# Performance work log

Measured on AMD Instinct MI355X. Metric: run time of the kernel, lower is better.

## Reference

```python
import jax, jax.numpy as jnp
import numpy as np

EMBED_DIM = 256
NUM_HEADS = 8
NB = 8          # number of scenes (batches)
LQ = 256        # queries per scene
LS = 4096       # source points per scene
LN_EPS = 1e-5


def setup_inputs() -> dict:
    key = jax.random.key(0)
    ks = jax.random.split(key, 8)
    d = EMBED_DIM
    n_q, n_s = NB * LQ, NB * LS
    w_scale = d ** -0.5  # xavier-ish
    return {
        "source": jax.random.normal(ks[0], (n_s, d), jnp.float32),
        "query": jax.random.normal(ks[1], (n_q, d), jnp.float32),
        "source_pe": 0.1 * jax.random.normal(ks[2], (n_s, d), jnp.float32),
        "query_pe": 0.1 * jax.random.normal(ks[3], (n_q, d), jnp.float32),
        "in_proj_w": w_scale * jax.random.normal(ks[4], (3 * d, d), jnp.float32),
        "in_proj_b": jnp.zeros((3 * d,), jnp.float32),
        "out_w": w_scale * jax.random.normal(ks[5], (d, d), jnp.float32),
        "out_b": jnp.zeros((d,), jnp.float32),
        "ln_w": jnp.ones((d,), jnp.float32),
        "ln_b": jnp.zeros((d,), jnp.float32),
        # sorted equal-size segments: token i belongs to scene i // L
        "source_batch": (jnp.arange(n_s, dtype=jnp.int32) // LS).astype(jnp.int32),
        "query_batch": (jnp.arange(n_q, dtype=jnp.int32) // LQ).astype(jnp.int32),
        "B": NB,
    }


def reference(source, query, source_pe, query_pe, in_proj_w, in_proj_b,
              out_w, out_b, ln_w, ln_b, source_batch, query_batch, B):
    d = source.shape[-1]
    H = NUM_HEADS
    hd = d // H
    Lq = query.shape[0] // B
    Ls = source.shape[0] // B

    # batch ids are sorted equal segments -> per-scene gather == reshape
    q_in = (query + query_pe).reshape(B, Lq, d)   # q with pos embed
    k_in = (source + source_pe).reshape(B, Ls, d) # k with pos embed
    v_in = source.reshape(B, Ls, d)               # v without pos embed

    Wq, Wk, Wv = jnp.split(in_proj_w, 3, axis=0)
    bq, bk, bv = jnp.split(in_proj_b, 3)

    q = (q_in @ Wq.T + bq).reshape(B, Lq, H, hd)
    k = (k_in @ Wk.T + bk).reshape(B, Ls, H, hd)
    v = (v_in @ Wv.T + bv).reshape(B, Ls, H, hd)

    scores = jnp.einsum('bqhd,bkhd->bhqk', q, k) * (hd ** -0.5)
    attn = jax.nn.softmax(scores, axis=-1)
    o = jnp.einsum('bhqk,bkhd->bqhd', attn, v).reshape(B, Lq, d)
    o = o @ out_w.T + out_b

    # residual (dropout is identity at p=0) + LayerNorm
    res = o + query.reshape(B, Lq, d)
    mu = jnp.mean(res, axis=-1, keepdims=True)
    var = jnp.var(res, axis=-1, keepdims=True)
    y = (res - mu) * jax.lax.rsqrt(var + LN_EPS) * ln_w + ln_b
    return y.reshape(-1, d)
```

## Files before the change

kernel.cpp:

```cpp
#include <hip/hip_runtime.h>
#include <hip/hip_bf16.h>

typedef __bf16 bf16;
typedef __bf16 bf16x4 __attribute__((ext_vector_type(4)));
typedef __bf16 bf16x8 __attribute__((ext_vector_type(8)));
typedef float f32x4 __attribute__((ext_vector_type(4)));

#define D 256
#define NHEAD 8
#define HD 32
#define NB_ 8
#define LQ_ 256
#define LS_ 4096
#define MQ (NB_ * LQ_)
#define MS (NB_ * LS_)

#define QSCALE 0.25500527f

__global__ __launch_bounds__(256) void prep(
    const float* __restrict__ source, const float* __restrict__ source_pe,
    const float* __restrict__ query, const float* __restrict__ query_pe,
    const float* __restrict__ w_in, const float* __restrict__ w_out,
    bf16* __restrict__ SPb, bf16* __restrict__ QPb, bf16* __restrict__ Wb)
{
    const int NS4 = MS * D / 4;
    const int NQ4 = MQ * D / 4;
    const int NW4 = (768 * 256 + 256 * 256) / 4;
    const int total = NS4 + NQ4 + NW4;
    for (int i = blockIdx.x * 256 + threadIdx.x; i < total; i += gridDim.x * 256) {
        if (i < NS4) {
            const float4 s = ((const float4*)source)[i];
            const float4 p = ((const float4*)source_pe)[i];
            bf16x4 osp;
            osp[0] = (bf16)(s.x + p.x); osp[1] = (bf16)(s.y + p.y);
            osp[2] = (bf16)(s.z + p.z); osp[3] = (bf16)(s.w + p.w);
            ((bf16x4*)SPb)[i] = osp;
        } else if (i < NS4 + NQ4) {
            const int j = i - NS4;
            const float4 s = ((const float4*)query)[j];
            const float4 p = ((const float4*)query_pe)[j];
            bf16x4 o;
            o[0] = (bf16)(s.x + p.x); o[1] = (bf16)(s.y + p.y);
            o[2] = (bf16)(s.z + p.z); o[3] = (bf16)(s.w + p.w);
            ((bf16x4*)QPb)[j] = o;
        } else {
            const int j = i - NS4 - NQ4;
            const float4 v = (j < 49152) ? ((const float4*)w_in)[j]
                                         : ((const float4*)w_out)[j - 49152];
            bf16x4 o;
            o[0] = (bf16)v.x; o[1] = (bf16)v.y; o[2] = (bf16)v.z; o[3] = (bf16)v.w;
            ((bf16x4*)Wb)[j] = o;
        }
    }
}

__global__ __launch_bounds__(256, 4) void gemm_proj(
    const bf16* __restrict__ SPb, const float* __restrict__ srcf,
    const bf16* __restrict__ QPb, const bf16* __restrict__ Wb,
    const float* __restrict__ in_proj_b,
    bf16* __restrict__ Kt, bf16* __restrict__ Vt2, bf16* __restrict__ Qb)
{
    __shared__ __align__(16) bf16 smem[2][128][72];
    bf16 (*As)[72] = smem[0];
    bf16 (*Bs)[72] = smem[1];
    const int tid = threadIdx.x, lane = tid & 63, wid = tid >> 6;
    const int wm = wid >> 1, wn = wid & 1;
    const int g = lane >> 4, q15 = lane & 15;
    const int id = blockIdx.x;

    const bf16* A; const bf16* W; const float* bias; bf16* out;
    int omode, mblk, nblk;
    if (id < 512) {
        A = SPb; W = Wb + 256 * D; bias = in_proj_b + 256; out = Kt;
        mblk = id >> 1; nblk = id & 1; omode = 1;
    } else if (id < 1024) {
        A = nullptr; W = Wb + 512 * D; bias = in_proj_b + 512; out = Vt2;
        mblk = (id - 512) >> 1; nblk = id & 1; omode = 2;
    } else {
        A = QPb; W = Wb; bias = in_proj_b; out = Qb;
        mblk = (id - 1024) >> 1; nblk = id & 1; omode = 0;
    }

    f32x4 acc[4][4];
    #pragma unroll
    for (int i = 0; i < 4; ++i)
        #pragma unroll
        for (int j = 0; j < 4; ++j) acc[i][j] = (f32x4){0.f, 0.f, 0.f, 0.f};

    const size_t arow0 = (size_t)mblk * 128;
    const int brow0 = nblk * 128;

    for (int kk = 0; kk < 4; ++kk) {
        const int d0 = kk * 64;
        if (omode == 2) {
            #pragma unroll
            for (int i = 0; i < 8; ++i) {
                const int idx = i * 256 + tid;
                const int r = idx >> 4, c = (idx & 15) * 4;
                const float4 v = *(const float4*)&srcf[(arow0 + r) * D + d0 + c];
                bf16x4 o;
                o[0] = (bf16)v.x; o[1] = (bf16)v.y; o[2] = (bf16)v.z; o[3] = (bf16)v.w;
                *(bf16x4*)&As[r][c] = o;
            }
            #pragma unroll
            for (int i = 0; i < 4; ++i) {
                const int idx = i * 256 + tid;
                const int r = idx >> 3, c = (idx & 7) * 8;
                *(bf16x8*)&Bs[r][c] = *(const bf16x8*)&W[(size_t)(brow0 + r) * D + d0 + c];
            }
        } else {
            #pragma unroll
            for (int i = 0; i < 4; ++i) {
                const int idx = i * 256 + tid;
                const int r = idx >> 3, c = (idx & 7) * 8;
                *(bf16x8*)&As[r][c] = *(const bf16x8*)&A[(arow0 + r) * D + d0 + c];
                *(bf16x8*)&Bs[r][c] = *(const bf16x8*)&W[(size_t)(brow0 + r) * D + d0 + c];
            }
        }
        __syncthreads();
        #pragma unroll
        for (int h2 = 0; h2 < 2; ++h2) {
            const int ko = h2 * 32 + g * 8;
            bf16x8 af[4], bfr[4];
            #pragma unroll
            for (int i = 0; i < 4; ++i)
                af[i] = *(const bf16x8*)&As[wm * 64 + i * 16 + q15][ko];
            #pragma unroll
            for (int j = 0; j < 4; ++j)
                bfr[j] = *(const bf16x8*)&Bs[wn * 64 + j * 16 + q15][ko];
            #pragma unroll
            for (int i = 0; i < 4; ++i)
                #pragma unroll
                for (int j = 0; j < 4; ++j)
                    acc[i][j] = __builtin_amdgcn_mfma_f32_16x16x32_bf16(
                        af[i], bfr[j], acc[i][j], 0, 0, 0);
        }
        __syncthreads();
    }

    if (omode == 0) {
        #pragma unroll
        for (int i = 0; i < 4; ++i)
            #pragma unroll
            for (int j = 0; j < 4; ++j) {
                const int n_g = nblk * 128 + wn * 64 + j * 16 + q15;
                const float b = bias[n_g];
                #pragma unroll
                for (int r = 0; r < 4; ++r) {
                    const size_t m_g = arow0 + wm * 64 + i * 16 + g * 4 + r;
                    out[m_g * D + n_g] = (bf16)((acc[i][j][r] + b) * QSCALE);
                }
            }
    } else if (omode == 1) {
        bf16* Ls = &smem[0][0][0];
        #pragma unroll
        for (int i = 0; i < 4; ++i)
            #pragma unroll
            for (int j = 0; j < 4; ++j) {
                const int n_loc = wn * 64 + j * 16 + q15;
                const int h_loc = n_loc >> 5, d = n_loc & 31;
                const int gp = d >> 3, e = d & 7;
                const float b = bias[nblk * 128 + n_loc];
                #pragma unroll
                for (int r = 0; r < 4; ++r) {
                    const int m_loc = wm * 64 + i * 16 + g * 4 + r;
                    const int c_loc = m_loc >> 6, kl = m_loc & 63;
                    const int t = ((kl >> 5) << 1) | ((kl >> 2) & 1);
                    const int q15p = ((kl >> 3) & 3) * 4 + (kl & 3);
                    Ls[(h_loc * 2 + c_loc) * 2048 + t * 512
                       + (gp * 16 + q15p) * 8 + e] = (bf16)(acc[i][j][r] + b);
                }
            }
        __syncthreads();
        const int bb = (int)(arow0 >> 12);
        const int c0 = (int)((arow0 & 4095) >> 6);
        const int h0 = (nblk * 128) >> 5;
        #pragma unroll
        for (int p = 0; p < 8; ++p) {
            const int idx = p * 2048 + tid * 8;
            const int blk = idx >> 11, within = idx & 2047;
            *(bf16x8*)&out[((size_t)(bb * 8 + h0 + (blk >> 1)) * 64
                            + c0 + (blk & 1)) * 2048 + within]
                = *(const bf16x8*)&Ls[idx];
        }
    } else {
        #pragma unroll
        for (int i = 0; i < 4; ++i)
            #pragma unroll
            for (int j = 0; j < 4; ++j) {
                const int n_g = nblk * 128 + wn * 64 + j * 16 + q15;
                const int h = n_g >> 5, d = n_g & 31;
                const int dt = d >> 4, q15p = d & 15;
                const float b = bias[n_g];
                const size_t m_g0 = arow0 + wm * 64 + i * 16 + g * 4;
                const int bb = (int)(m_g0 >> 12);
                const int c = (int)((m_g0 & 4095) >> 6);
                const int kl0 = (int)(m_g0 & 63);
                const int half = kl0 >> 5, gp = (kl0 >> 3) & 3, e0 = kl0 & 7;
                const int f = dt * 2 + half;
                bf16x4 o;
                #pragma unroll
                for (int r = 0; r < 4; ++r) o[r] = (bf16)(acc[i][j][r] + b);
                *(bf16x4*)&out[((size_t)(bb * 8 + h) * 64 + c) * 2048
                               + f * 512 + (gp * 16 + q15p) * 8 + e0] = o;
            }
    }
}

template<int S>
__global__ __launch_bounds__(256, 2) void attn_kernel(
    const bf16* __restrict__ Qb, const bf16* __restrict__ Kt,
    const bf16* __restrict__ Vt2,
    bf16* __restrict__ accp, float* __restrict__ lp)
{
    const int tid = threadIdx.x, lane = tid & 63, wid = tid >> 6;
    const int q15 = lane & 15, g = lane >> 4;
    const int bid = blockIdx.x;
    const int h = bid & 7;
    const int inner = bid >> 3;
    const int split = inner % S;
    const int b = inner / S;
    constexpr int CHUNKS = LS_ / S / 64;

    const int q0 = b * LQ_ + wid * 64;
    bf16x8 qf[4];
    #pragma unroll
    for (int f = 0; f < 4; ++f)
        qf[f] = *(const bf16x8*)&Qb[(size_t)(q0 + f * 16 + q15) * D + h * HD + g * 8];

    const f32x4 minit = (f32x4){-8.f, -8.f, -8.f, -8.f};
    const size_t cbase = ((size_t)(b * 8 + h) * 64 + split * CHUNKS) * 2048;
    const bf16* kp = Kt + cbase + lane * 8;
    const bf16* vp = Vt2 + cbase + lane * 8;

    float lr[4] = {0.f, 0.f, 0.f, 0.f};
    f32x4 a0[4], a1[4];
    #pragma unroll
    for (int f = 0; f < 4; ++f) {
        a0[f] = (f32x4){0.f, 0.f, 0.f, 0.f};
        a1[f] = (f32x4){0.f, 0.f, 0.f, 0.f};
    }

    for (int kc = 0; kc < CHUNKS; ++kc) {
        const size_t co = (size_t)kc * 2048;

        bf16x8 kf[4], vf[4];
        #pragma unroll
        for (int t = 0; t < 4; ++t) kf[t] = *(const bf16x8*)&kp[co + t * 512];
        #pragma unroll
        for (int t = 0; t < 4; ++t) vf[t] = *(const bf16x8*)&vp[co + t * 512];

        #pragma unroll
        for (int f = 0; f < 4; ++f) {
            f32x4 s0 = __builtin_amdgcn_mfma_f32_16x16x32_bf16(kf[0], qf[f], minit, 0, 0, 0);
            f32x4 s1 = __builtin_amdgcn_mfma_f32_16x16x32_bf16(kf[1], qf[f], minit, 0, 0, 0);
            f32x4 s2 = __builtin_amdgcn_mfma_f32_16x16x32_bf16(kf[2], qf[f], minit, 0, 0, 0);
            f32x4 s3 = __builtin_amdgcn_mfma_f32_16x16x32_bf16(kf[3], qf[f], minit, 0, 0, 0);

            bf16x8 pa0, pa1;
            #pragma unroll
            for (int r = 0; r < 4; ++r) {
                const float p0 = exp2f(s0[r]);
                const float p1 = exp2f(s1[r]);
                const float p2 = exp2f(s2[r]);
                const float p3 = exp2f(s3[r]);
                lr[f] += (p0 + p1) + (p2 + p3);
                pa0[r]     = (bf16)p0;
                pa0[4 + r] = (bf16)p1;
                pa1[r]     = (bf16)p2;
                pa1[4 + r] = (bf16)p3;
            }

            a0[f] = __builtin_amdgcn_mfma_f32_16x16x32_bf16(pa0, vf[0], a0[f], 0, 0, 0);
            a0[f] = __builtin_amdgcn_mfma_f32_16x16x32_bf16(pa1, vf[1], a0[f], 0, 0, 0);
            a1[f] = __builtin_amdgcn_mfma_f32_16x16x32_bf16(pa0, vf[2], a1[f], 0, 0, 0);
            a1[f] = __builtin_amdgcn_mfma_f32_16x16x32_bf16(pa1, vf[3], a1[f], 0, 0, 0);
        }
    }

    const int task0 = (b * 8 + h) * 16 + wid * 4;
    #pragma unroll
    for (int f = 0; f < 4; ++f) {
        lr[f] += __shfl_xor(lr[f], 16);
        lr[f] += __shfl_xor(lr[f], 32);
        const size_t base = ((size_t)((task0 + f) * S + split) * 64 + lane) * 8;
        bf16x4 o0, o1;
        #pragma unroll
        for (int r = 0; r < 4; ++r) {
            o0[r] = (bf16)a0[f][r];
            o1[r] = (bf16)a1[f][r];
        }
        *(bf16x4*)&accp[base]     = o0;
        *(bf16x4*)&accp[base + 4] = o1;
        if (lane < 16)
            lp[((task0 + f) * S + split) * 16 + lane] = lr[f];
    }
}

template<int S>
__global__ __launch_bounds__(256) void attn_combine(
    const bf16* __restrict__ accp, const float* __restrict__ lp,
    bf16* __restrict__ Ob)
{
    const int tid = threadIdx.x, lane = tid & 63, wid = tid >> 6;
    const int task = blockIdx.x * 4 + wid;
    const int g = lane >> 4, q15 = lane & 15;

    f32x4 o0 = (f32x4){0.f, 0.f, 0.f, 0.f};
    f32x4 o1 = (f32x4){0.f, 0.f, 0.f, 0.f};
    float ll = 0.f;
    #pragma unroll
    for (int s = 0; s < S; ++s) {
        const size_t base = ((size_t)(task * S + s) * 64 + lane) * 8;
        const bf16x8 v = *(const bf16x8*)&accp[base];
        #pragma unroll
        for (int r = 0; r < 4; ++r) { o0[r] += (float)v[r]; o1[r] += (float)v[4 + r]; }
        if (lane < 16) ll += lp[(task * S + s) * 16 + lane];
    }

    const int b = task >> 7, h = (task >> 4) & 7, qg = task & 15;
    #pragma unroll
    for (int r = 0; r < 4; ++r) {
        const float inv = 1.f / __shfl(ll, g * 4 + r);
        const size_t row = (size_t)b * LQ_ + qg * 16 + g * 4 + r;
        Ob[row * D + h * HD + q15]      = (bf16)(o0[r] * inv);
        Ob[row * D + h * HD + 16 + q15] = (bf16)(o1[r] * inv);
    }
}

__global__ __launch_bounds__(256) void out_ln_kernel(
    const bf16* __restrict__ Ob, const bf16* __restrict__ Wout,
    const float* __restrict__ out_b, const float* __restrict__ query,
    const float* __restrict__ lnw, const float* __restrict__ lnb,
    float* __restrict__ out)
{
    __shared__ bf16 As[32][72];
    __shared__ bf16 Bs[256][72];
    __shared__ float red[2][32][2];
    const int tid = threadIdx.x, lane = tid & 63, wid = tid >> 6;
    const int wm = wid >> 1, wn = wid & 1;
    const int g = lane >> 4, q15 = lane & 15;
    const size_t row0 = (size_t)blockIdx.x * 32;

    f32x4 acc[8];
    #pragma unroll
    for (int j = 0; j < 8; ++j) acc[j] = (f32x4){0.f, 0.f, 0.f, 0.f};

    for (int kk = 0; kk < 4; ++kk) {
        const int d0 = kk * 64;
        {
            const int r = tid >> 3, c = (tid & 7) * 8;
            *(bf16x8*)&As[r][c] = *(const bf16x8*)&Ob[(row0 + r) * D + d0 + c];
        }
        #pragma unroll
        for (int i = 0; i < 8; ++i) {
            const int idx = i * 256 + tid;
            const int r = idx >> 3, c = (idx & 7) * 8;
            *(bf16x8*)&Bs[r][c] = *(const bf16x8*)&Wout[(size_t)r * D + d0 + c];
        }
        __syncthreads();
        #pragma unroll
        for (int h2 = 0; h2 < 2; ++h2) {
            const int ko = h2 * 32 + g * 8;
            const bf16x8 af = *(const bf16x8*)&As[wm * 16 + q15][ko];
            #pragma unroll
            for (int j = 0; j < 8; ++j) {
                const bf16x8 bfr = *(const bf16x8*)&Bs[wn * 128 + j * 16 + q15][ko];
                acc[j] = __builtin_amdgcn_mfma_f32_16x16x32_bf16(af, bfr, acc[j], 0, 0, 0);
            }
        }
        __syncthreads();
    }

    float bl[8], lw[8], lbv[8];
    #pragma unroll
    for (int j = 0; j < 8; ++j) {
        const int n = wn * 128 + j * 16 + q15;
        bl[j] = out_b[n]; lw[j] = lnw[n]; lbv[j] = lnb[n];
    }

    #pragma unroll
    for (int r = 0; r < 4; ++r) {
        const int rl = wm * 16 + g * 4 + r;
        const size_t m = row0 + rl;
        float s = 0.f, sq = 0.f;
        #pragma unroll
        for (int j = 0; j < 8; ++j) {
            const float v = acc[j][r] + bl[j] + query[m * D + wn * 128 + j * 16 + q15];
            acc[j][r] = v;
            s += v; sq += v * v;
        }
        s += __shfl_xor(s, 1);  sq += __shfl_xor(sq, 1);
        s += __shfl_xor(s, 2);  sq += __shfl_xor(sq, 2);
        s += __shfl_xor(s, 4);  sq += __shfl_xor(sq, 4);
        s += __shfl_xor(s, 8);  sq += __shfl_xor(sq, 8);
        if (q15 == r) {
            red[wn][rl][0] = s;
            red[wn][rl][1] = sq;
        }
    }
    __syncthreads();

    #pragma unroll
    for (int r = 0; r < 4; ++r) {
        const int rl = wm * 16 + g * 4 + r;
        const float s  = red[0][rl][0] + red[1][rl][0];
        const float sq = red[0][rl][1] + red[1][rl][1];
        const float mean = s * (1.f / 256.f);
        const float var  = sq * (1.f / 256.f) - mean * mean;
        const float inv  = rsqrtf(var + 1e-5f);
        const size_t m = row0 + rl;
        #pragma unroll
        for (int j = 0; j < 8; ++j)
            out[m * D + wn * 128 + j * 16 + q15] =
                (acc[j][r] - mean) * inv * lw[j] + lbv[j];
    }
}

extern "C" void kernel_launch(void* const* d_in, const int* in_sizes, int n_in,
                              void* d_out, int out_size, void* d_ws, size_t ws_size,
                              hipStream_t stream) {
    (void)in_sizes; (void)n_in; (void)out_size; (void)ws_size;
    const float* source    = (const float*)d_in[0];
    const float* query     = (const float*)d_in[1];
    const float* source_pe = (const float*)d_in[2];
    const float* query_pe  = (const float*)d_in[3];
    const float* in_proj_w = (const float*)d_in[4];
    const float* in_proj_b = (const float*)d_in[5];
    const float* out_w     = (const float*)d_in[6];
    const float* out_b     = (const float*)d_in[7];
    const float* ln_w      = (const float*)d_in[8];
    const float* ln_b      = (const float*)d_in[9];

    constexpr int S = 8;
    bf16* Wb   = (bf16*)d_ws;
    bf16* QPb  = Wb + 1024 * 256;
    bf16* Qb   = QPb + (size_t)MQ * D;
    bf16* Kt   = Qb + (size_t)MQ * D;
    bf16* Vt2  = Kt + (size_t)MS * D;
    bf16* SPb  = Vt2 + (size_t)MS * D;
    bf16* Ob   = SPb + (size_t)MS * D;
    bf16* accp = Ob + (size_t)MQ * D;
    float* lp  = (float*)(accp + (size_t)1024 * S * 64 * 8);
    float* outp = (float*)d_out;

    prep<<<dim3(2048), dim3(256), 0, stream>>>(
        source, source_pe, query, query_pe, in_proj_w, out_w,
        SPb, QPb, Wb);
    gemm_proj<<<dim3(1056), dim3(256), 0, stream>>>(
        SPb, source, QPb, Wb, in_proj_b, Kt, Vt2, Qb);
    attn_kernel<S><<<dim3(512), dim3(256), 0, stream>>>(Qb, Kt, Vt2, accp, lp);
    attn_combine<S><<<dim3(256), dim3(256), 0, stream>>>(accp, lp, Ob);
    out_ln_kernel<<<dim3(64), dim3(256), 0, stream>>>(
        Ob, Wb + 768 * 256, out_b, query, ln_w, ln_b, outp);
}
```

Measured before the change: 82.27 us.

## Compute softmax row sums via MFMA and double attention key splits

The softmax denominator is now accumulated with extra MFMAs against a ones vector, replacing per-element VALU adds and the cross-lane shuffle reduction. The key-split count goes from 8 to 16, doubling the attention grid. The occupancy hint in launch bounds is raised from 2 to 4. The aim is more parallelism and less VALU pressure in the exp loop. In exchange there is more MFMA work per chunk, more partial results for the combine kernel to read, and tighter register limits that could cause spills.

```diff
diff --git a/kernel.cpp b/kernel.cpp
--- a/kernel.cpp
+++ b/kernel.cpp
@@ -208,7 +208,7 @@
 }
 
 template<int S>
-__global__ __launch_bounds__(256, 2) void attn_kernel(
+__global__ __launch_bounds__(256, 4) void attn_kernel(
     const bf16* __restrict__ Qb, const bf16* __restrict__ Kt,
     const bf16* __restrict__ Vt2,
     bf16* __restrict__ accp, float* __restrict__ lp)
@@ -229,16 +229,20 @@
         qf[f] = *(const bf16x8*)&Qb[(size_t)(q0 + f * 16 + q15) * D + h * HD + g * 8];
 
     const f32x4 minit = (f32x4){-8.f, -8.f, -8.f, -8.f};
+    bf16x8 ones;
+    #pragma unroll
+    for (int e = 0; e < 8; ++e) ones[e] = (bf16)1.0f;
+
     const size_t cbase = ((size_t)(b * 8 + h) * 64 + split * CHUNKS) * 2048;
     const bf16* kp = Kt + cbase + lane * 8;
     const bf16* vp = Vt2 + cbase + lane * 8;
 
-    float lr[4] = {0.f, 0.f, 0.f, 0.f};
-    f32x4 a0[4], a1[4];
+    f32x4 a0[4], a1[4], al[4];
     #pragma unroll
     for (int f = 0; f < 4; ++f) {
         a0[f] = (f32x4){0.f, 0.f, 0.f, 0.f};
         a1[f] = (f32x4){0.f, 0.f, 0.f, 0.f};
+        al[f] = (f32x4){0.f, 0.f, 0.f, 0.f};
     }
 
     for (int kc = 0; kc < CHUNKS; ++kc) {
@@ -260,29 +264,24 @@
             bf16x8 pa0, pa1;
             #pragma unroll
             for (int r = 0; r < 4; ++r) {
-                const float p0 = exp2f(s0[r]);
-                const float p1 = exp2f(s1[r]);
-                const float p2 = exp2f(s2[r]);
-                const float p3 = exp2f(s3[r]);
-                lr[f] += (p0 + p1) + (p2 + p3);
-                pa0[r]     = (bf16)p0;
-                pa0[4 + r] = (bf16)p1;
-                pa1[r]     = (bf16)p2;
-                pa1[4 + r] = (bf16)p3;
+                pa0[r]     = (bf16)exp2f(s0[r]);
+                pa0[4 + r] = (bf16)exp2f(s1[r]);
+                pa1[r]     = (bf16)exp2f(s2[r]);
+                pa1[4 + r] = (bf16)exp2f(s3[r]);
             }
 
             a0[f] = __builtin_amdgcn_mfma_f32_16x16x32_bf16(pa0, vf[0], a0[f], 0, 0, 0);
             a0[f] = __builtin_amdgcn_mfma_f32_16x16x32_bf16(pa1, vf[1], a0[f], 0, 0, 0);
             a1[f] = __builtin_amdgcn_mfma_f32_16x16x32_bf16(pa0, vf[2], a1[f], 0, 0, 0);
             a1[f] = __builtin_amdgcn_mfma_f32_16x16x32_bf16(pa1, vf[3], a1[f], 0, 0, 0);
+            al[f] = __builtin_amdgcn_mfma_f32_16x16x32_bf16(pa0, ones,  al[f], 0, 0, 0);
+            al[f] = __builtin_amdgcn_mfma_f32_16x16x32_bf16(pa1, ones,  al[f], 0, 0, 0);
         }
     }
 
     const int task0 = (b * 8 + h) * 16 + wid * 4;
     #pragma unroll
     for (int f = 0; f < 4; ++f) {
-        lr[f] += __shfl_xor(lr[f], 16);
-        lr[f] += __shfl_xor(lr[f], 32);
         const size_t base = ((size_t)((task0 + f) * S + split) * 64 + lane) * 8;
         bf16x4 o0, o1;
         #pragma unroll
@@ -292,8 +291,11 @@
         }
         *(bf16x4*)&accp[base]     = o0;
         *(bf16x4*)&accp[base + 4] = o1;
-        if (lane < 16)
-            lp[((task0 + f) * S + split) * 16 + lane] = lr[f];
+        if (q15 == 0) {
+            #pragma unroll
+            for (int r = 0; r < 4; ++r)
+                lp[((task0 + f) * S + split) * 16 + g * 4 + r] = al[f][r];
+        }
     }
 }
 
@@ -432,7 +434,7 @@
     const float* ln_w      = (const float*)d_in[8];
     const float* ln_b      = (const float*)d_in[9];
 
-    constexpr int S = 8;
+    constexpr int S = 16;
     bf16* Wb   = (bf16*)d_ws;
     bf16* QPb  = Wb + 1024 * 256;
     bf16* Qb   = QPb + (size_t)MQ * D;
@@ -449,7 +451,7 @@
         SPb, QPb, Wb);
     gemm_proj<<<dim3(1056), dim3(256), 0, stream>>>(
         SPb, source, QPb, Wb, in_proj_b, Kt, Vt2, Qb);
-    attn_kernel<S><<<dim3(512), dim3(256), 0, stream>>>(Qb, Kt, Vt2, accp, lp);
+    attn_kernel<S><<<dim3(NB_ * S * 8), dim3(256), 0, stream>>>(Qb, Kt, Vt2, accp, lp);
     attn_combine<S><<<dim3(256), dim3(256), 0, stream>>>(accp, lp, Ob);
     out_ln_kernel<<<dim3(64), dim3(256), 0, stream>>>(
         Ob, Wb + 768 * 256, out_b, query, ln_w, ln_b, outp);
```

Measured after the change: 84.94 us. +3.2%, slower.
